# Kernel optimization log

Hardware: AMD Instinct MI355X
Metric: run time of the kernel (lower is better)

## Reference

```python
import jax, jax.numpy as jnp
import numpy as np

GAMMA = 2.0
EPS = 1e-06
LAMBDA_DISTANCE = 1.0
LAMBDA_NORMAL = 0.01
LAMBDA_LAPLACIAN = 0.1
CLS = 1


def vertex_normals(v, f, eps=EPS):
    # v: [N,3], f: [F,3] int. Scatter face normals to vertices, then normalize.
    fv = v[f]  # [F,3,3]
    fn = jnp.cross(fv[:, 1] - fv[:, 0], fv[:, 2] - fv[:, 0])  # [F,3]
    vn = jnp.zeros_like(v)
    vn = vn.at[f[:, 0]].add(fn).at[f[:, 1]].add(fn).at[f[:, 2]].add(fn)
    norm = jnp.maximum(jnp.linalg.norm(vn, axis=-1, keepdims=True), eps)
    return vn / norm


def squared_cdist(a, b):
    # [Na,3] x [Nb,3] -> squared euclidean distances [Na,Nb] (clamped >= 0)
    a2 = jnp.sum(a * a, axis=1)[:, None]
    b2 = jnp.sum(b * b, axis=1)[None, :]
    d2 = a2 + b2 - 2.0 * (a @ b.T)
    return jnp.maximum(d2, 0.0)


def sample_binary_targets(label, v, cls=CLS):
    # Nearest-neighbor grid_sample, align_corners=True, padding zeros.
    # grid = 2*v - 1 -> voxel index = round(v * (size-1)); v[:,0]->W, v[:,1]->H, v[:,2]->D.
    D, H, W = label.shape[2], label.shape[3], label.shape[4]
    ix = jnp.round(v[:, 0] * (W - 1)).astype(jnp.int32)
    iy = jnp.round(v[:, 1] * (H - 1)).astype(jnp.int32)
    iz = jnp.round(v[:, 2] * (D - 1)).astype(jnp.int32)
    inb = (ix >= 0) & (ix < W) & (iy >= 0) & (iy < H) & (iz >= 0) & (iz < D)
    ixc = jnp.clip(ix, 0, W - 1)
    iyc = jnp.clip(iy, 0, H - 1)
    izc = jnp.clip(iz, 0, D - 1)
    vals = (label[0, 0, izc, iyc, ixc] == cls).astype(jnp.float32)
    return jnp.where(inb, vals, 0.0)


def spatial_consistency_loss(rel_pos, targets, gamma=GAMMA, eps=EPS):
    p = jnp.clip(rel_pos, eps, 1.0 - eps)
    pos = targets > 0.5
    pc = jnp.sum(pos).astype(p.dtype)
    tot = jnp.asarray(p.shape[0], p.dtype)
    nc = tot - pc
    alpha = nc / (tot + eps)
    lpos = -alpha * jnp.power(1.0 - p, gamma) * jnp.log(p)
    lneg = -(1.0 - alpha) * jnp.power(p, gamma) * jnp.log(1.0 - p)
    return jnp.sum(jnp.where(pos, lpos, lneg)) / (tot + eps)


def laplacian_uniform(v, f):
    # Uniform mesh Laplacian smoothing: || mean(neighbors) - v ||, averaged.
    i = jnp.concatenate([f[:, 0], f[:, 1], f[:, 2], f[:, 1], f[:, 2], f[:, 0]])
    j = jnp.concatenate([f[:, 1], f[:, 2], f[:, 0], f[:, 0], f[:, 1], f[:, 2]])
    nsum = jnp.zeros_like(v).at[i].add(v[j])
    deg = jnp.zeros((v.shape[0],), v.dtype).at[i].add(1.0)
    lap = nsum / jnp.maximum(deg, 1.0)[:, None] - v
    return jnp.mean(jnp.linalg.norm(lap, axis=1))


def loss_forward(pred_vertices, relative_positions, gt_vertices, pred_faces, gt_faces, label):
    gt_v = jax.lax.stop_gradient(gt_vertices)  # gt comes from label volume; detached in original
    gt_normals = vertex_normals(gt_v, gt_faces)
    # spatial (focal-style) loss
    targets = sample_binary_targets(label, pred_vertices)
    spatial = spatial_consistency_loss(relative_positions, targets)
    # chamfer-style squared surface distance
    d2 = squared_cdist(pred_vertices, gt_v)  # [Np,Ng]
    distance = jnp.mean(jnp.min(d2, axis=1)) + jnp.mean(jnp.min(d2, axis=0))
    # normal consistency vs nearest gt vertex
    pred_normals = vertex_normals(pred_vertices, pred_faces)
    nearest = jnp.argmin(d2, axis=1)
    normal = jnp.mean((pred_normals - gt_normals[nearest]) ** 2)
    # uniform laplacian smoothing
    laplacian = laplacian_uniform(pred_vertices, pred_faces)
    total = spatial + LAMBDA_DISTANCE * distance + LAMBDA_NORMAL * normal + LAMBDA_LAPLACIAN * laplacian
    return total


def setup_inputs() -> dict:
    key = jax.random.key(0)
    k1, k2, k3, k4, k5, k6 = jax.random.split(key, 6)
    Np, Ng = 8192, 12000
    pred_vertices = jax.random.uniform(k1, (Np, 3), dtype=jnp.float32)
    relative_positions = jax.random.uniform(k2, (Np,), dtype=jnp.float32)
    gt_vertices = jax.random.uniform(k3, (Ng, 3), dtype=jnp.float32)
    pred_faces = jax.random.randint(k4, (2 * Np, 3), 0, Np, dtype=jnp.int32)
    gt_faces = jax.random.randint(k5, (2 * Ng, 3), 0, Ng, dtype=jnp.int32)
    label = jax.random.randint(k6, (1, 1, 96, 96, 96), 0, 2, dtype=jnp.int32)
    return {"pred_vertices": pred_vertices, "relative_positions": relative_positions,
            "gt_vertices": gt_vertices, "pred_faces": pred_faces,
            "gt_faces": gt_faces, "label": label}


def reference(pred_vertices, relative_positions, gt_vertices, pred_faces, gt_faces, label):
    return loss_forward(pred_vertices, relative_positions, gt_vertices, pred_faces, gt_faces, label)
```

## Files before the change

kernel.cpp:

```cpp
#include <hip/hip_runtime.h>
#include <math.h>

#define NP 8192
#define NG 12000
#define NFP 16384
#define NFG 24000
#define EPSF 1e-6f

#define GR 16
#define NC (GR*GR*GR)
#define HCELL 0.0625f

#define N_ZERO 101545
#define ZERO_BLOCKS ((N_ZERO + 1023) / 1024)
#define D1_BLOCKS (2 + ZERO_BLOCKS)

#define PQB64 (NP / 64)
#define GQB64 ((NG + 63) / 64)
#define FQB64 ((NFG + NFP + 63) / 64)
#define D2_BLOCKS (PQB64 + GQB64 + FQB64)

#define FIN_BLOCKS (NP / 256)

static constexpr size_t OFF_STARTP = 0;
static constexpr size_t OFF_STARTG = 16640;
static constexpr size_t OFF_SORTP  = 33280;
static constexpr size_t OFF_SORTG  = 164352;
static constexpr size_t OFF_GTN    = 356352;
static constexpr size_t OFF_PNN    = 500352;
static constexpr size_t OFF_NSUM   = 598656;
static constexpr size_t OFF_DEG    = 696960;
static constexpr size_t OFF_NEAR   = 729728;
static constexpr size_t OFF_ACCUM  = 762496;
static constexpr size_t OFF_DONE   = 762528;

__device__ __forceinline__ int cell_of(float x) {
    int c = (int)(x * (float)GR);
    return min(max(c, 0), GR - 1);
}

__device__ __forceinline__ void build_cells(const float* __restrict__ pts, int n,
                                            unsigned* __restrict__ start,
                                            float4* __restrict__ sorted,
                                            unsigned* h, unsigned* wsum) {
    int t = threadIdx.x;
    int lane = t & 63, wid = t >> 6;
    for (int i = t; i < NC; i += 1024) h[i] = 0u;
    __syncthreads();
    for (int i = t; i < n; i += 1024) {
        int c = (cell_of(pts[3*i+2]) * GR + cell_of(pts[3*i+1])) * GR + cell_of(pts[3*i]);
        atomicAdd(&h[c], 1u);
    }
    __syncthreads();
    unsigned a0 = h[4*t], a1 = h[4*t+1], a2 = h[4*t+2], a3 = h[4*t+3];
    unsigned tsum = a0 + a1 + a2 + a3;
    unsigned x = tsum;
    #pragma unroll
    for (int off = 1; off < 64; off <<= 1) {
        unsigned y = __shfl_up(x, off, 64);
        if (lane >= off) x += y;
    }
    if (lane == 63) wsum[wid] = x;
    __syncthreads();
    if (t < 16) {
        unsigned w = wsum[t];
        #pragma unroll
        for (int off = 1; off < 16; off <<= 1) {
            unsigned y = __shfl_up(w, off, 64);
            if (t >= off) w += y;
        }
        wsum[t] = w;
    }
    __syncthreads();
    unsigned base = (wid ? wsum[wid-1] : 0u) + (x - tsum);
    unsigned e0 = base, e1 = base + a0, e2 = base + a0 + a1, e3 = base + a0 + a1 + a2;
    start[4*t] = e0; start[4*t+1] = e1; start[4*t+2] = e2; start[4*t+3] = e3;
    h[4*t] = e0; h[4*t+1] = e1; h[4*t+2] = e2; h[4*t+3] = e3;
    __syncthreads();
    for (int i = t; i < n; i += 1024) {
        float px = pts[3*i], py = pts[3*i+1], pz = pts[3*i+2];
        int c = (cell_of(pz) * GR + cell_of(py)) * GR + cell_of(px);
        unsigned pos = atomicAdd(&h[c], 1u);
        sorted[pos] = make_float4(px, py, pz, __int_as_float(i));
    }
    if (t == 0) start[NC] = (unsigned)n;
}

__global__ __launch_bounds__(1024) void build_kernel(const float* __restrict__ pred,
                                                     const float* __restrict__ gt,
                                                     unsigned* __restrict__ startP,
                                                     unsigned* __restrict__ startG,
                                                     float4* __restrict__ sortP,
                                                     float4* __restrict__ sortG,
                                                     float* __restrict__ zero) {
    __shared__ unsigned h[NC];
    __shared__ unsigned wsum[16];
    if (blockIdx.x == 0) {
        build_cells(pred, NP, startP, sortP, h, wsum);
    } else if (blockIdx.x == 1) {
        build_cells(gt, NG, startG, sortG, h, wsum);
    } else {
        int i = (blockIdx.x - 2) * 1024 + threadIdx.x;
        if (i < N_ZERO) zero[i] = 0.0f;
    }
}

__device__ __forceinline__ float wave_sum(float x) {
    #pragma unroll
    for (int o = 32; o > 0; o >>= 1) x += __shfl_down(x, o, 64);
    return x;
}

__device__ __forceinline__ unsigned long long u64min(unsigned long long a,
                                                     unsigned long long b) {
    return a < b ? a : b;
}

__device__ __forceinline__ unsigned long long pack_key(float px, float py, float pz,
                                                       float4 q) {
    float ddx = px - q.x, ddy = py - q.y, ddz = pz - q.z;
    float d2 = fmaf(ddx, ddx, fmaf(ddy, ddy, ddz*ddz));
    return ((unsigned long long)__float_as_uint(d2) << 32) |
           (unsigned)__float_as_int(q.w);
}

__device__ unsigned long long lane_nn(float px, float py, float pz,
                                      const float4* __restrict__ S,
                                      const unsigned* __restrict__ cstart) {
    int cx = cell_of(px), cy = cell_of(py), cz = cell_of(pz);
    unsigned long long best = 0xFFFFFFFFFFFFFFFFULL;
    {
        int x0 = max(cx - 1, 0), x1 = min(cx + 1, GR - 1);
        #pragma unroll
        for (int dz = -1; dz <= 1; ++dz) {
            #pragma unroll
            for (int dy = -1; dy <= 1; ++dy) {
                int z = cz + dz, y = cy + dy;
                if (z >= 0 && z < GR && y >= 0 && y < GR) {
                    int rowbase = (z * GR + y) * GR;
                    unsigned s0 = cstart[rowbase + x0];
                    unsigned s1 = cstart[rowbase + x1 + 1];
                    for (unsigned u = s0; u < s1; ++u)
                        best = u64min(best, pack_key(px, py, pz, S[u]));
                }
            }
        }
        bool covered = (cx - 1 <= 0) & (cx + 1 >= GR - 1) &
                       (cy - 1 <= 0) & (cy + 1 >= GR - 1) &
                       (cz - 1 <= 0) & (cz + 1 >= GR - 1);
        float blo = 1.0e30f;
        if (cx - 1 > 0)      blo = fminf(blo, px - (float)(cx - 1) * HCELL);
        if (cx + 1 < GR - 1) blo = fminf(blo, (float)(cx + 2) * HCELL - px);
        if (cy - 1 > 0)      blo = fminf(blo, py - (float)(cy - 1) * HCELL);
        if (cy + 1 < GR - 1) blo = fminf(blo, (float)(cy + 2) * HCELL - py);
        if (cz - 1 > 0)      blo = fminf(blo, pz - (float)(cz - 1) * HCELL);
        if (cz + 1 < GR - 1) blo = fminf(blo, (float)(cz + 2) * HCELL - pz);
        float bd2 = __uint_as_float((unsigned)(best >> 32));
        if (covered || (bd2 <= blo * blo)) return best;
    }
    for (int r = 2; ; ++r) {
        int x0 = max(cx - r, 0), x1 = min(cx + r, GR - 1);
        int y0 = max(cy - r, 0), y1 = min(cy + r, GR - 1);
        int z0 = max(cz - r, 0), z1 = min(cz + r, GR - 1);
        for (int z = z0; z <= z1; ++z) {
            for (int y = y0; y <= y1; ++y) {
                int rowbase = (z * GR + y) * GR;
                unsigned s0 = cstart[rowbase + x0];
                unsigned s1 = cstart[rowbase + x1 + 1];
                for (unsigned u = s0; u < s1; ++u)
                    best = u64min(best, pack_key(px, py, pz, S[u]));
            }
        }
        bool covered = (x0 == 0) & (x1 == GR-1) & (y0 == 0) &
                       (y1 == GR-1) & (z0 == 0) & (z1 == GR-1);
        if (covered) break;
        float blo = 1.0e30f;
        if (cx - r > 0)      blo = fminf(blo, px - (float)(cx - r) * HCELL);
        if (cx + r < GR - 1) blo = fminf(blo, (float)(cx + r + 1) * HCELL - px);
        if (cy - r > 0)      blo = fminf(blo, py - (float)(cy - r) * HCELL);
        if (cy + r < GR - 1) blo = fminf(blo, (float)(cy + r + 1) * HCELL - py);
        if (cz - r > 0)      blo = fminf(blo, pz - (float)(cz - r) * HCELL);
        if (cz + r < GR - 1) blo = fminf(blo, (float)(cz + r + 1) * HCELL - pz);
        float bd2 = __uint_as_float((unsigned)(best >> 32));
        if (bd2 <= blo * blo) break;
    }
    return best;
}

__global__ __launch_bounds__(64) void work_kernel(const float* __restrict__ pred,
                                                  const int* __restrict__ pf,
                                                  const float* __restrict__ gt,
                                                  const int* __restrict__ gf,
                                                  const float4* __restrict__ sortP,
                                                  const float4* __restrict__ sortG,
                                                  const unsigned* __restrict__ startP,
                                                  const unsigned* __restrict__ startG,
                                                  float* __restrict__ gtn,
                                                  float* __restrict__ pnn,
                                                  float* __restrict__ nsum,
                                                  float* __restrict__ deg,
                                                  int* __restrict__ nearestIdx,
                                                  float* __restrict__ accum) {
    int b = blockIdx.x, t = threadIdx.x;
    if (b < PQB64) {
        int qid = b * 64 + t;
        float4 P = sortP[qid];
        unsigned long long key = lane_nn(P.x, P.y, P.z, sortG, startG);
        int v = __float_as_int(P.w);
        nearestIdx[v] = (int)(unsigned)(key & 0xffffffffu);
        float r0 = wave_sum(__uint_as_float((unsigned)(key >> 32)));
        if (t == 0) atomicAdd(&accum[0], r0);
    } else if (b < PQB64 + GQB64) {
        int qid = (b - PQB64) * 64 + t;
        float r0 = 0.0f;
        if (qid < NG) {
            float4 Q = sortG[qid];
            unsigned long long key = lane_nn(Q.x, Q.y, Q.z, sortP, startP);
            r0 = __uint_as_float((unsigned)(key >> 32));
        }
        r0 = wave_sum(r0);
        if (t == 0) atomicAdd(&accum[6], r0);
    } else {
        int f = (b - PQB64 - GQB64) * 64 + t;
        if (f < NFG) {
            int i0 = gf[3*f], i1 = gf[3*f+1], i2 = gf[3*f+2];
            float ax = gt[3*i0], ay = gt[3*i0+1], az = gt[3*i0+2];
            float bx = gt[3*i1], by = gt[3*i1+1], bz = gt[3*i1+2];
            float cx = gt[3*i2], cy = gt[3*i2+1], cz = gt[3*i2+2];
            float ux = bx-ax, uy = by-ay, uz = bz-az;
            float wx = cx-ax, wy = cy-ay, wz = cz-az;
            float nx = uy*wz - uz*wy, ny = uz*wx - ux*wz, nz = ux*wy - uy*wx;
            atomicAdd(&gtn[3*i0+0], nx); atomicAdd(&gtn[3*i0+1], ny); atomicAdd(&gtn[3*i0+2], nz);
            atomicAdd(&gtn[3*i1+0], nx); atomicAdd(&gtn[3*i1+1], ny); atomicAdd(&gtn[3*i1+2], nz);
            atomicAdd(&gtn[3*i2+0], nx); atomicAdd(&gtn[3*i2+1], ny); atomicAdd(&gtn[3*i2+2], nz);
        } else if (f < NFG + NFP) {
            int u = f - NFG;
            int i0 = pf[3*u], i1 = pf[3*u+1], i2 = pf[3*u+2];
            float ax = pred[3*i0], ay = pred[3*i0+1], az = pred[3*i0+2];
            float bx = pred[3*i1], by = pred[3*i1+1], bz = pred[3*i1+2];
            float cx = pred[3*i2], cy = pred[3*i2+1], cz = pred[3*i2+2];
            float ux = bx-ax, uy = by-ay, uz = bz-az;
            float wx = cx-ax, wy = cy-ay, wz = cz-az;
            float nx = uy*wz - uz*wy, ny = uz*wx - ux*wz, nz = ux*wy - uy*wx;
            atomicAdd(&pnn[3*i0+0], nx); atomicAdd(&pnn[3*i0+1], ny); atomicAdd(&pnn[3*i0+2], nz);
            atomicAdd(&pnn[3*i1+0], nx); atomicAdd(&pnn[3*i1+1], ny); atomicAdd(&pnn[3*i1+2], nz);
            atomicAdd(&pnn[3*i2+0], nx); atomicAdd(&pnn[3*i2+1], ny); atomicAdd(&pnn[3*i2+2], nz);
            atomicAdd(&nsum[3*i0+0], bx+cx); atomicAdd(&nsum[3*i0+1], by+cy); atomicAdd(&nsum[3*i0+2], bz+cz);
            atomicAdd(&nsum[3*i1+0], cx+ax); atomicAdd(&nsum[3*i1+1], cy+ay); atomicAdd(&nsum[3*i1+2], cz+az);
            atomicAdd(&nsum[3*i2+0], ax+bx); atomicAdd(&nsum[3*i2+1], ay+by); atomicAdd(&nsum[3*i2+2], az+bz);
            atomicAdd(&deg[i0], 2.0f); atomicAdd(&deg[i1], 2.0f); atomicAdd(&deg[i2], 2.0f);
        }
    }
}

__global__ __launch_bounds__(256) void finish_kernel(const float* __restrict__ pred,
                                                     const float* __restrict__ relpos,
                                                     const int* __restrict__ label,
                                                     const float* __restrict__ pnn,
                                                     const float* __restrict__ gtn,
                                                     const float* __restrict__ nsum,
                                                     const float* __restrict__ deg,
                                                     const int* __restrict__ nearestIdx,
                                                     float* __restrict__ accum,
                                                     unsigned* __restrict__ done,
                                                     float* __restrict__ out) {
    int v = blockIdx.x * 256 + threadIdx.x;
    float px = pred[3*v], py = pred[3*v+1], pz = pred[3*v+2];
    int nearest = nearestIdx[v];

    float ax = pnn[3*v], ay = pnn[3*v+1], az = pnn[3*v+2];
    float an = fmaxf(sqrtf(ax*ax + ay*ay + az*az), EPSF);
    float gx = gtn[3*nearest], gy = gtn[3*nearest+1], gz = gtn[3*nearest+2];
    float gn = fmaxf(sqrtf(gx*gx + gy*gy + gz*gz), EPSF);
    float nx = ax/an - gx/gn, ny = ay/an - gy/gn, nz = az/an - gz/gn;
    float sse = nx*nx + ny*ny + nz*nz;

    float d = fmaxf(deg[v], 1.0f);
    float lx = nsum[3*v]/d - px, ly = nsum[3*v+1]/d - py, lz = nsum[3*v+2]/d - pz;
    float lapn = sqrtf(lx*lx + ly*ly + lz*lz);

    int ix = (int)rintf(px * 95.0f), iy = (int)rintf(py * 95.0f), iz = (int)rintf(pz * 95.0f);
    bool inb = (ix >= 0) & (ix < 96) & (iy >= 0) & (iy < 96) & (iz >= 0) & (iz < 96);
    int ixc = min(max(ix, 0), 95), iyc = min(max(iy, 0), 95), izc = min(max(iz, 0), 95);
    bool pos = inb && (label[(izc*96 + iyc)*96 + ixc] == 1);

    float p = fminf(fmaxf(relpos[v], EPSF), 1.0f - EPSF);
    float om = 1.0f - p;
    float pcnt = 0.0f, sx = 0.0f, sy = 0.0f;
    if (pos) { pcnt = 1.0f; sx = om*om*logf(p); }
    else     { sy = p*p*logf(om); }

    float r1 = wave_sum(sse), r2 = wave_sum(lapn), r3 = wave_sum(pcnt);
    float r4 = wave_sum(sx),  r5 = wave_sum(sy);
    __shared__ float bsum[5];
    __shared__ bool isLast;
    if (threadIdx.x < 5) bsum[threadIdx.x] = 0.0f;
    __syncthreads();
    if ((threadIdx.x & 63) == 0) {
        atomicAdd(&bsum[0], r1); atomicAdd(&bsum[1], r2); atomicAdd(&bsum[2], r3);
        atomicAdd(&bsum[3], r4); atomicAdd(&bsum[4], r5);
    }
    __syncthreads();
    if (threadIdx.x == 0) {
        atomicAdd(&accum[1], bsum[0]); atomicAdd(&accum[2], bsum[1]);
        atomicAdd(&accum[3], bsum[2]); atomicAdd(&accum[4], bsum[3]);
        atomicAdd(&accum[5], bsum[4]);
        __threadfence();
        unsigned prev = atomicAdd(done, 1u);
        isLast = (prev == FIN_BLOCKS - 1);
    }
    __syncthreads();
    if (isLast && threadIdx.x == 0) {
        __threadfence();
        float sum_row = __hip_atomic_load(&accum[0], __ATOMIC_RELAXED, __HIP_MEMORY_SCOPE_AGENT);
        float sse_t   = __hip_atomic_load(&accum[1], __ATOMIC_RELAXED, __HIP_MEMORY_SCOPE_AGENT);
        float lap_t   = __hip_atomic_load(&accum[2], __ATOMIC_RELAXED, __HIP_MEMORY_SCOPE_AGENT);
        float pc      = __hip_atomic_load(&accum[3], __ATOMIC_RELAXED, __HIP_MEMORY_SCOPE_AGENT);
        float SX      = __hip_atomic_load(&accum[4], __ATOMIC_RELAXED, __HIP_MEMORY_SCOPE_AGENT);
        float SY      = __hip_atomic_load(&accum[5], __ATOMIC_RELAXED, __HIP_MEMORY_SCOPE_AGENT);
        float sum_col = __hip_atomic_load(&accum[6], __ATOMIC_RELAXED, __HIP_MEMORY_SCOPE_AGENT);
        float tot = (float)NP;
        float alpha = (tot - pc) / (tot + EPSF);
        float spatial = (-alpha * SX - (1.0f - alpha) * SY) / (tot + EPSF);
        float distance = sum_row / (float)NP + sum_col / (float)NG;
        float normal = sse_t / (float)(NP * 3);
        float lapm = lap_t / (float)NP;
        out[0] = spatial + 1.0f * distance + 0.01f * normal + 0.1f * lapm;
    }
}

extern "C" void kernel_launch(void* const* d_in, const int* in_sizes, int n_in,
                              void* d_out, int out_size, void* d_ws, size_t ws_size,
                              hipStream_t stream) {
    const float* pred   = (const float*)d_in[0];
    const float* relpos = (const float*)d_in[1];
    const float* gt     = (const float*)d_in[2];
    const int*   pfaces = (const int*)d_in[3];
    const int*   gfaces = (const int*)d_in[4];
    const int*   label  = (const int*)d_in[5];
    float* out = (float*)d_out;

    char* ws = (char*)d_ws;
    unsigned* startP  = (unsigned*)(ws + OFF_STARTP);
    unsigned* startG  = (unsigned*)(ws + OFF_STARTG);
    float4*   sortP   = (float4*)(ws + OFF_SORTP);
    float4*   sortG   = (float4*)(ws + OFF_SORTG);
    float*    gtn     = (float*)(ws + OFF_GTN);
    float*    pnn     = (float*)(ws + OFF_PNN);
    float*    nsum    = (float*)(ws + OFF_NSUM);
    float*    deg     = (float*)(ws + OFF_DEG);
    int*      nearest = (int*)(ws + OFF_NEAR);
    float*    accum   = (float*)(ws + OFF_ACCUM);
    unsigned* done    = (unsigned*)(ws + OFF_DONE);

    hipLaunchKernelGGL(build_kernel, dim3(D1_BLOCKS), dim3(1024), 0, stream,
                       pred, gt, startP, startG, sortP, sortG,
                       (float*)(ws + OFF_GTN));
    hipLaunchKernelGGL(work_kernel, dim3(D2_BLOCKS), dim3(64), 0, stream,
                       pred, pfaces, gt, gfaces, sortP, sortG, startP, startG,
                       gtn, pnn, nsum, deg, nearest, accum);
    hipLaunchKernelGGL(finish_kernel, dim3(FIN_BLOCKS), dim3(256), 0, stream,
                       pred, relpos, label, pnn, gtn, nsum, deg, nearest,
                       accum, done, out);
}
```

Measured before the change: 144.0 us.

## Cooperative 16-lane NN search with shared-memory staging of candidate z-slab

Each query is now handled by a group of 16 lanes that split the neighbouring cell rows and combine their results with an xor-shuffle min. Blocks grow to 1024 threads (64 queries each). Before the first ring search, each block copies the sorted points and cell starts for the z-slab its queries cover into LDS. The change targets lane divergence and scattered global gathers in the per-lane grid search, at the cost of a large LDS footprint, lower occupancy, extra barriers, and falling back to global memory for wide slabs and outer rings.

```diff
diff --git a/kernel.cpp b/kernel.cpp
--- a/kernel.cpp
+++ b/kernel.cpp
@@ -10,15 +10,20 @@
 #define GR 16
 #define NC (GR*GR*GR)
 #define HCELL 0.0625f
+#define QL 16
 
 #define N_ZERO 101545
 #define ZERO_BLOCKS ((N_ZERO + 1023) / 1024)
 #define D1_BLOCKS (2 + ZERO_BLOCKS)
 
-#define PQB64 (NP / 64)
-#define GQB64 ((NG + 63) / 64)
-#define FQB64 ((NFG + NFP + 63) / 64)
-#define D2_BLOCKS (PQB64 + GQB64 + FQB64)
+#define QPBLK 64
+#define PQB (NP / QPBLK)
+#define GQB ((NG + QPBLK - 1) / QPBLK)
+#define FB  ((NFG + NFP + 1023) / 1024)
+#define D2_BLOCKS (PQB + GQB + FB)
+
+#define CAPP  4608
+#define CWCAP 1312
 
 #define FIN_BLOCKS (NP / 256)
 
@@ -124,27 +129,37 @@
            (unsigned)__float_as_int(q.w);
 }
 
-__device__ unsigned long long lane_nn(float px, float py, float pz,
-                                      const float4* __restrict__ S,
-                                      const unsigned* __restrict__ cstart) {
+__device__ unsigned long long group_nn(int lane, float px, float py, float pz,
+                                       const float4* __restrict__ Sg,
+                                       const unsigned* __restrict__ CSg,
+                                       const float4* Sl, const unsigned* CSl,
+                                       int c_lo, unsigned p_lo, bool staged) {
     int cx = cell_of(px), cy = cell_of(py), cz = cell_of(pz);
     unsigned long long best = 0xFFFFFFFFFFFFFFFFULL;
     {
         int x0 = max(cx - 1, 0), x1 = min(cx + 1, GR - 1);
-        #pragma unroll
-        for (int dz = -1; dz <= 1; ++dz) {
-            #pragma unroll
-            for (int dy = -1; dy <= 1; ++dy) {
-                int z = cz + dz, y = cy + dy;
-                if (z >= 0 && z < GR && y >= 0 && y < GR) {
-                    int rowbase = (z * GR + y) * GR;
-                    unsigned s0 = cstart[rowbase + x0];
-                    unsigned s1 = cstart[rowbase + x1 + 1];
+        unsigned long long lb = 0xFFFFFFFFFFFFFFFFULL;
+        for (int k = lane; k < 9; k += QL) {
+            int z = cz + k / 3 - 1, y = cy + k % 3 - 1;
+            if (z >= 0 && z < GR && y >= 0 && y < GR) {
+                int rowbase = (z * GR + y) * GR;
+                if (staged) {
+                    unsigned s0 = CSl[rowbase + x0 - c_lo];
+                    unsigned s1 = CSl[rowbase + x1 + 1 - c_lo];
                     for (unsigned u = s0; u < s1; ++u)
-                        best = u64min(best, pack_key(px, py, pz, S[u]));
+                        lb = u64min(lb, pack_key(px, py, pz, Sl[u - p_lo]));
+                } else {
+                    unsigned s0 = CSg[rowbase + x0];
+                    unsigned s1 = CSg[rowbase + x1 + 1];
+                    for (unsigned u = s0; u < s1; ++u)
+                        lb = u64min(lb, pack_key(px, py, pz, Sg[u]));
                 }
             }
         }
+        best = lb;
+        #pragma unroll
+        for (int m = 1; m < QL; m <<= 1)
+            best = u64min(best, (unsigned long long)__shfl_xor((long long)best, m, 64));
         bool covered = (cx - 1 <= 0) & (cx + 1 >= GR - 1) &
                        (cy - 1 <= 0) & (cy + 1 >= GR - 1) &
                        (cz - 1 <= 0) & (cz + 1 >= GR - 1);
@@ -159,20 +174,27 @@
         if (covered || (bd2 <= blo * blo)) return best;
     }
     for (int r = 2; ; ++r) {
+        int w = 2 * r + 1;
+        int nrows = w * w;
         int x0 = max(cx - r, 0), x1 = min(cx + r, GR - 1);
-        int y0 = max(cy - r, 0), y1 = min(cy + r, GR - 1);
-        int z0 = max(cz - r, 0), z1 = min(cz + r, GR - 1);
-        for (int z = z0; z <= z1; ++z) {
-            for (int y = y0; y <= y1; ++y) {
+        unsigned long long lb = 0xFFFFFFFFFFFFFFFFULL;
+        for (int k = lane; k < nrows; k += QL) {
+            int z = cz + k / w - r, y = cy + k % w - r;
+            if (z >= 0 && z < GR && y >= 0 && y < GR) {
                 int rowbase = (z * GR + y) * GR;
-                unsigned s0 = cstart[rowbase + x0];
-                unsigned s1 = cstart[rowbase + x1 + 1];
+                unsigned s0 = CSg[rowbase + x0];
+                unsigned s1 = CSg[rowbase + x1 + 1];
                 for (unsigned u = s0; u < s1; ++u)
-                    best = u64min(best, pack_key(px, py, pz, S[u]));
+                    lb = u64min(lb, pack_key(px, py, pz, Sg[u]));
             }
         }
-        bool covered = (x0 == 0) & (x1 == GR-1) & (y0 == 0) &
-                       (y1 == GR-1) & (z0 == 0) & (z1 == GR-1);
+        best = u64min(best, lb);
+        #pragma unroll
+        for (int m = 1; m < QL; m <<= 1)
+            best = u64min(best, (unsigned long long)__shfl_xor((long long)best, m, 64));
+        bool covered = (cx - r <= 0) & (cx + r >= GR - 1) &
+                       (cy - r <= 0) & (cy + r >= GR - 1) &
+                       (cz - r <= 0) & (cz + r >= GR - 1);
         if (covered) break;
         float blo = 1.0e30f;
         if (cx - r > 0)      blo = fminf(blo, px - (float)(cx - r) * HCELL);
@@ -187,41 +209,78 @@
     return best;
 }
 
-__global__ __launch_bounds__(64) void work_kernel(const float* __restrict__ pred,
-                                                  const int* __restrict__ pf,
-                                                  const float* __restrict__ gt,
-                                                  const int* __restrict__ gf,
-                                                  const float4* __restrict__ sortP,
-                                                  const float4* __restrict__ sortG,
-                                                  const unsigned* __restrict__ startP,
-                                                  const unsigned* __restrict__ startG,
-                                                  float* __restrict__ gtn,
-                                                  float* __restrict__ pnn,
-                                                  float* __restrict__ nsum,
-                                                  float* __restrict__ deg,
-                                                  int* __restrict__ nearestIdx,
-                                                  float* __restrict__ accum) {
+__global__ __launch_bounds__(1024) void work_kernel(const float* __restrict__ pred,
+                                                    const int* __restrict__ pf,
+                                                    const float* __restrict__ gt,
+                                                    const int* __restrict__ gf,
+                                                    const float4* __restrict__ sortP,
+                                                    const float4* __restrict__ sortG,
+                                                    const unsigned* __restrict__ startP,
+                                                    const unsigned* __restrict__ startG,
+                                                    float* __restrict__ gtn,
+                                                    float* __restrict__ pnn,
+                                                    float* __restrict__ nsum,
+                                                    float* __restrict__ deg,
+                                                    int* __restrict__ nearestIdx,
+                                                    float* __restrict__ accum) {
+    __shared__ float4 lpts[CAPP];
+    __shared__ unsigned lcs[CWCAP];
+    __shared__ float qacc;
+    __shared__ int s_info[4];
     int b = blockIdx.x, t = threadIdx.x;
-    if (b < PQB64) {
-        int qid = b * 64 + t;
-        float4 P = sortP[qid];
-        unsigned long long key = lane_nn(P.x, P.y, P.z, sortG, startG);
-        int v = __float_as_int(P.w);
-        nearestIdx[v] = (int)(unsigned)(key & 0xffffffffu);
-        float r0 = wave_sum(__uint_as_float((unsigned)(key >> 32)));
-        if (t == 0) atomicAdd(&accum[0], r0);
-    } else if (b < PQB64 + GQB64) {
-        int qid = (b - PQB64) * 64 + t;
+
+    if (b < PQB + GQB) {
+        bool is_pred = (b < PQB);
+        const float4*   Q  = is_pred ? sortP  : sortG;
+        const float4*   S  = is_pred ? sortG  : sortP;
+        const unsigned* CS = is_pred ? startG : startP;
+        int qbase = (is_pred ? b : (b - PQB)) * QPBLK;
+        int nq = min(QPBLK, (is_pred ? NP : NG) - qbase);
+
+        if (t == 0) {
+            qacc = 0.0f;
+            float4 qf = Q[qbase], ql = Q[qbase + nq - 1];
+            int z_lo = cell_of(qf.z), z_hi = cell_of(ql.z);
+            int c_lo  = max(z_lo - 1, 0) * (GR * GR);
+            int c_end = min(z_hi + 2, GR) * (GR * GR);
+            int cw = c_end - c_lo + 1;
+            unsigned p_lo = CS[c_lo], p_hi = CS[c_end];
+            int np = (int)(p_hi - p_lo);
+            bool ok = (cw <= CWCAP) && (np <= CAPP);
+            s_info[0] = c_lo; s_info[1] = (int)p_lo; s_info[2] = np;
+            s_info[3] = ok ? cw : -cw;
+        }
+        __syncthreads();
+        int c_lo = s_info[0];
+        unsigned p_lo = (unsigned)s_info[1];
+        int np = s_info[2];
+        int cw = s_info[3];
+        bool staged = (cw > 0);
+        if (staged) {
+            for (int i = t; i < np; i += 1024) lpts[i] = S[p_lo + i];
+            for (int i = t; i < cw; i += 1024) lcs[i]  = CS[c_lo + i];
+        }
+        __syncthreads();
+
+        int lane = t & (QL - 1), group = t >> 4;
         float r0 = 0.0f;
-        if (qid < NG) {
-            float4 Q = sortG[qid];
-            unsigned long long key = lane_nn(Q.x, Q.y, Q.z, sortP, startP);
-            r0 = __uint_as_float((unsigned)(key >> 32));
+        if (group < nq) {
+            int qid = qbase + group;
+            float4 P = Q[qid];
+            unsigned long long key = group_nn(lane, P.x, P.y, P.z, S, CS,
+                                              lpts, lcs, c_lo, p_lo, staged);
+            if (lane == 0) {
+                r0 = __uint_as_float((unsigned)(key >> 32));
+                if (is_pred)
+                    nearestIdx[__float_as_int(P.w)] = (int)(unsigned)(key & 0xffffffffu);
+            }
         }
         r0 = wave_sum(r0);
-        if (t == 0) atomicAdd(&accum[6], r0);
+        if ((t & 63) == 0) atomicAdd(&qacc, r0);
+        __syncthreads();
+        if (t == 0) atomicAdd(&accum[is_pred ? 0 : 6], qacc);
     } else {
-        int f = (b - PQB64 - GQB64) * 64 + t;
+        int f = (b - PQB - GQB) * 1024 + t;
         if (f < NFG) {
             int i0 = gf[3*f], i1 = gf[3*f+1], i2 = gf[3*f+2];
             float ax = gt[3*i0], ay = gt[3*i0+1], az = gt[3*i0+2];
@@ -356,7 +415,7 @@
     hipLaunchKernelGGL(build_kernel, dim3(D1_BLOCKS), dim3(1024), 0, stream,
                        pred, gt, startP, startG, sortP, sortG,
                        (float*)(ws + OFF_GTN));
-    hipLaunchKernelGGL(work_kernel, dim3(D2_BLOCKS), dim3(64), 0, stream,
+    hipLaunchKernelGGL(work_kernel, dim3(D2_BLOCKS), dim3(1024), 0, stream,
                        pred, pfaces, gt, gfaces, sortP, sortG, startP, startG,
                        gtn, pnn, nsum, deg, nearest, accum);
     hipLaunchKernelGGL(finish_kernel, dim3(FIN_BLOCKS), dim3(256), 0, stream,
```

After: 132.2 us. 1.09x faster.
